# Kernel optimization log

Measured on AMD Instinct MI355X. Metric: run time of the kernel, lower is better.

Reference implementation:

```python
import jax, jax.numpy as jnp
import numpy as np

N = 100_000
E = 1_600_000
H = 128
F_NODE = 8
F_EDGE = 4
STEPS = 6
LN_EPS = 1e-6


def _ln(x, scale, bias):
    m = x.mean(-1, keepdims=True)
    v = ((x - m) ** 2).mean(-1, keepdims=True)
    return (x - m) * jax.lax.rsqrt(v + LN_EPS) * scale + bias


def setup_inputs() -> dict:
    key = jax.random.key(0)
    ks = iter(jax.random.split(key, 40))

    def rn(shape, scale=0.05):
        return jax.random.normal(next(ks), shape, jnp.float32) * scale

    inp = dict(
        node_feats=jax.random.normal(next(ks), (N, F_NODE), jnp.float32),
        edge_index=jax.random.randint(next(ks), (2, E), 0, N, jnp.int32),
        edge_feats=jax.random.normal(next(ks), (E, F_EDGE), jnp.float32),
        # input projection
        W_in=rn((F_NODE, H)), b_in=jnp.zeros((H,), jnp.float32),
        # per-step message MLP (distinct params each mp step -> leading axis STEPS)
        W_m1=rn((STEPS, 2 * H + F_EDGE, H)), b_m1=jnp.zeros((STEPS, H), jnp.float32),
        W_m2=rn((STEPS, H, H)), b_m2=jnp.zeros((STEPS, H), jnp.float32),
        # per-step GRU-style gates
        W_z=rn((STEPS, 2 * H, H)), b_z=jnp.zeros((STEPS, H), jnp.float32),
        W_r=rn((STEPS, 2 * H, H)), b_r=jnp.zeros((STEPS, H), jnp.float32),
        W_h=rn((STEPS, 2 * H, H)), b_h=jnp.zeros((STEPS, H), jnp.float32),
        # per-step LayerNorm
        ln_scale=jnp.ones((STEPS, H), jnp.float32), ln_bias=jnp.zeros((STEPS, H), jnp.float32),
        # classification head
        W_c1=rn((H, 64)), b_c1=jnp.zeros((64,), jnp.float32),
        W_c2=rn((64, 5)), b_c2=jnp.zeros((5,), jnp.float32),
        # collapse probability head
        W_p1=rn((H, 64)), b_p1=jnp.zeros((64,), jnp.float32),
        W_p2=rn((64, 1)), b_p2=jnp.zeros((1,), jnp.float32),
    )
    return inp


def reference(node_feats, edge_index, edge_feats, W_in, b_in,
              W_m1, b_m1, W_m2, b_m2, W_z, b_z, W_r, b_r, W_h, b_h,
              ln_scale, ln_bias, W_c1, b_c1, W_c2, b_c2, W_p1, b_p1, W_p2, b_p2):
    src, dst = edge_index[0], edge_index[1]
    h = node_feats @ W_in + b_in  # [N, H]
    n = h.shape[0]
    for s in range(STEPS):
        msg_in = jnp.concatenate([h[src], h[dst], edge_feats], axis=-1)  # [E, 2H+4]
        msg = jax.nn.relu(msg_in @ W_m1[s] + b_m1[s]) @ W_m2[s] + b_m2[s]  # [E, H]
        agg = jnp.zeros((n, H), h.dtype).at[dst].add(msg)  # [N, H]
        gate_in = jnp.concatenate([h, agg], axis=-1)  # [N, 2H]
        z = jax.nn.sigmoid(gate_in @ W_z[s] + b_z[s])
        r = jax.nn.sigmoid(gate_in @ W_r[s] + b_r[s])
        h_new = jnp.tanh(jnp.concatenate([r * h, agg], axis=-1) @ W_h[s] + b_h[s])
        h = _ln((1 - z) * h + z * h_new, ln_scale[s], ln_bias[s])
    cls = jax.nn.relu(h @ W_c1 + b_c1) @ W_c2 + b_c2  # [N, 5]
    prob = jax.nn.sigmoid(jax.nn.relu(h @ W_p1 + b_p1) @ W_p2 + b_p2).squeeze(-1)  # [N]
    return cls, prob
```

## Files before the change

kernel.cpp:

```cpp
#include <hip/hip_runtime.h>

#define STEPS 6

typedef __attribute__((ext_vector_type(8))) short short8;
typedef __attribute__((ext_vector_type(4))) float f32x4;
typedef __attribute__((ext_vector_type(8))) float f32x8;

__device__ __forceinline__ float bf2f(unsigned int u16) {
    union { unsigned int u; float f; } v; v.u = u16 << 16; return v.f;
}
__device__ __forceinline__ unsigned int f2bf(float x) {
    union { float f; unsigned int u; } v; v.f = x;
    unsigned int r = v.u + 0x7fffu + ((v.u >> 16) & 1u);
    return r >> 16;
}
__device__ __forceinline__ void decompv(const f32x8& v, short8& hi, short8& lo) {
#pragma unroll
    for (int j = 0; j < 8; ++j) {
        float x = v[j];
        unsigned int h = f2bf(x);
        hi[j] = (short)h;
        lo[j] = (short)f2bf(x - bf2f(h));
    }
}
__device__ __forceinline__ void gl_lds16(const void* g, void* s) {
    __builtin_amdgcn_global_load_lds(
        (const __attribute__((address_space(1))) unsigned int*)g,
        (__attribute__((address_space(3))) unsigned int*)s, 16, 0, 0);
}

__global__ __launch_bounds__(256) void hist_k(const int* __restrict__ dst, int* __restrict__ deg, int E) {
    int e = blockIdx.x * 256 + threadIdx.x;
    if (e < E) atomicAdd(&deg[dst[e]], 1);
}

__global__ __launch_bounds__(256) void scan1_k(const int* __restrict__ in, int* __restrict__ ex,
                                               int* __restrict__ bs, int N) {
    __shared__ int sd[256];
    int t = threadIdx.x;
    int base = blockIdx.x * 1024 + t * 4;
    int v[4]; int s = 0;
#pragma unroll
    for (int i = 0; i < 4; ++i) { int idx = base + i; v[i] = idx < N ? in[idx] : 0; s += v[i]; }
    sd[t] = s; __syncthreads();
    for (int o = 1; o < 256; o <<= 1) {
        int x = (t >= o) ? sd[t - o] : 0;
        __syncthreads();
        sd[t] += x;
        __syncthreads();
    }
    int run = sd[t] - s;
#pragma unroll
    for (int i = 0; i < 4; ++i) { int idx = base + i; if (idx < N) ex[idx] = run; run += v[i]; }
    if (t == 255) bs[blockIdx.x] = sd[255];
}

__global__ __launch_bounds__(1024) void scan2_k(const int* __restrict__ bs, int* __restrict__ be, int nb) {
    __shared__ int sd[1024];
    int t = threadIdx.x;
    int v = (t < nb) ? bs[t] : 0;
    sd[t] = v; __syncthreads();
    for (int o = 1; o < 1024; o <<= 1) {
        int x = (t >= o) ? sd[t - o] : 0;
        __syncthreads();
        sd[t] += x;
        __syncthreads();
    }
    if (t < nb) be[t] = sd[t] - v;
}

__global__ __launch_bounds__(256) void scan3_k(const int* __restrict__ ex, const int* __restrict__ be,
                                               int* __restrict__ offs, int N, int E) {
    int i = blockIdx.x * 256 + threadIdx.x;
    if (i < N) offs[i] = ex[i] + be[i >> 10];
    if (i == N) offs[N] = E;
}

__global__ __launch_bounds__(256) void scatter_k(const int* __restrict__ src, const int* __restrict__ dst,
                                                 const float4* __restrict__ ef,
                                                 const int* __restrict__ offs,
                                                 int* __restrict__ cursor, int* __restrict__ src_sorted,
                                                 uint2* __restrict__ ef16_sorted, int E) {
    int e = blockIdx.x * 256 + threadIdx.x;
    if (e >= E) return;
    int d = dst[e];
    int pos = offs[d] + atomicAdd(&cursor[d], 1);
    src_sorted[pos] = src[e];
    float4 f = ef[e];
    uint2 p;
    p.x = f2bf(f.x) | (f2bf(f.y) << 16);
    p.y = f2bf(f.z) | (f2bf(f.w) << 16);
    ef16_sorted[pos] = p;
}

__global__ __launch_bounds__(256) void pack_k(const float* __restrict__ W_m1, const float* __restrict__ W_m2,
                                              const float* __restrict__ W_z, const float* __restrict__ W_r,
                                              const float* __restrict__ W_h, unsigned short* __restrict__ packed) {
    const int s = blockIdx.y, mat = blockIdx.z;
    const int t = blockIdx.x * 256 + threadIdx.x;
    const int lane = t & 63;
    int KS, width; size_t moff;
    if (mat == 0)      { KS = 4; width = 256; moff = 0; }
    else if (mat == 1) { KS = 4; width = 128; moff = 32768; }
    else if (mat == 2) { KS = 8; width = 128; moff = 49152; }
    else if (mat == 3) { KS = 8; width = 128; moff = 81920; }
    else               { KS = 8; width = 128; moff = 114688; }
    const int total = (width >> 4) * KS * 64;
    if (t >= total) return;
    const int ks = (t >> 6) % KS;
    const int ct = (t >> 6) / KS;
    const int col = ct * 16 + (lane & 15);
    const int kb = ks * 32 + (lane >> 4) * 8;
    unsigned short* dh = packed + (size_t)s * 294912 + moff;
    unsigned short* dl = dh + 147456;
#pragma unroll
    for (int j = 0; j < 8; ++j) {
        const int k = kb + j;
        float v;
        if (mat == 0) {
            const float* W = W_m1 + (size_t)s * 260 * 128;
            v = (col < 128) ? W[k * 128 + col] : W[(128 + k) * 128 + (col - 128)];
        } else if (mat == 1) {
            v = W_m2[(size_t)s * 16384 + k * 128 + col];
        } else if (mat == 2) {
            v = W_z[(size_t)s * 32768 + k * 128 + col];
        } else if (mat == 3) {
            v = W_r[(size_t)s * 32768 + k * 128 + col];
        } else {
            v = W_h[(size_t)s * 32768 + k * 128 + col];
        }
        unsigned int hb = f2bf(v);
        dh[(size_t)t * 8 + j] = (unsigned short)hb;
        dl[(size_t)t * 8 + j] = (unsigned short)f2bf(v - bf2f(hb));
    }
}

__global__ __launch_bounds__(256) void pack_head_k(const float* __restrict__ Wc1,
                                                   const float* __restrict__ Wp1,
                                                   unsigned short* __restrict__ dst) {
    const int t = blockIdx.x * 256 + threadIdx.x;
    if (t >= 2048) return;
    const int lane = t & 63;
    const int ks = (t >> 6) & 3;
    const int ct = (t >> 6) >> 2;
    const int col = ct * 16 + (lane & 15);
    const int kb = ks * 32 + (lane >> 4) * 8;
    unsigned short* dh = dst;
    unsigned short* dl = dst + 16384;
#pragma unroll
    for (int j = 0; j < 8; ++j) {
        const int k = kb + j;
        float v = (col < 64) ? Wc1[k * 64 + col] : Wp1[k * 64 + (col - 64)];
        unsigned int hb = f2bf(v);
        dh[(size_t)t * 8 + j] = (unsigned short)hb;
        dl[(size_t)t * 8 + j] = (unsigned short)f2bf(v - bf2f(hb));
    }
}

__global__ __launch_bounds__(256) void proj_k(const float* __restrict__ nf, const float* __restrict__ Win,
                                              const float* __restrict__ bin,
                                              float* __restrict__ hf, int N) {
    const int lane = threadIdx.x & 63, wave = threadIdx.x >> 6;
    const int i = blockIdx.x * 4 + wave;
    if (i >= N) return;
    const int c0 = lane * 2;
    float a0 = bin[c0], a1 = bin[c0 + 1];
#pragma unroll
    for (int q = 0; q < 8; ++q) {
        float x = nf[(size_t)i * 8 + q];
        a0 += x * Win[q * 128 + c0];
        a1 += x * Win[q * 128 + c0 + 1];
    }
    hf[(size_t)i * 128 + c0] = a0;
    hf[(size_t)i * 128 + c0 + 1] = a1;
}

template <int MODE>
__global__ __launch_bounds__(256, 4) void gemm_k(const float* __restrict__ A, int lda,
                                                 const unsigned short* __restrict__ pkh,
                                                 const unsigned short* __restrict__ pkl,
                                                 const float* __restrict__ bias,
                                                 const int* __restrict__ deg,
                                                 float* __restrict__ out, int ldo,
                                                 unsigned short* __restrict__ out_b,
                                                 int Nrows) {
    const int lane = threadIdx.x & 63;
    const int wave = threadIdx.x >> 6;
    const int l15 = lane & 15, l16 = lane >> 4;
    const int mrow = blockIdx.x * 64 + wave * 16;
    const int cgrp = blockIdx.y;

    int r0 = mrow + l15; if (r0 >= Nrows) r0 = 0;
    const float* ap = A + (size_t)r0 * lda;

    f32x4 acc[8];
#pragma unroll
    for (int ct = 0; ct < 8; ++ct) acc[ct] = (f32x4){0.f, 0.f, 0.f, 0.f};

    for (int ks = 0; ks < 4; ++ks) {
        const f32x8 av = *(const f32x8*)(ap + ks * 32 + l16 * 8);
        short8 ahi, alo;
        decompv(av, ahi, alo);
#pragma unroll
        for (int ct = 0; ct < 8; ++ct) {
            const size_t fb = (((size_t)(cgrp * 8 + ct) * 4 + ks) << 10) + lane * 16;
            const short8 wh = *(const short8*)((const char*)pkh + fb);
            const short8 wl = *(const short8*)((const char*)pkl + fb);
            acc[ct] = __builtin_amdgcn_mfma_f32_16x16x32_bf16(ahi, wh, acc[ct], 0, 0, 0);
            acc[ct] = __builtin_amdgcn_mfma_f32_16x16x32_bf16(alo, wh, acc[ct], 0, 0, 0);
            acc[ct] = __builtin_amdgcn_mfma_f32_16x16x32_bf16(ahi, wl, acc[ct], 0, 0, 0);
        }
    }
#pragma unroll
    for (int ct = 0; ct < 8; ++ct) {
        const int col = cgrp * 128 + ct * 16 + l15;
#pragma unroll
        for (int r = 0; r < 4; ++r) {
            const int row = mrow + l16 * 4 + r;
            if (row >= Nrows) continue;
            float v = acc[ct][r];
            if (MODE == 0) {
                if (cgrp == 0) out_b[(size_t)row * 128 + col] = (unsigned short)f2bf(v);
                else           out[(size_t)row * ldo + col] = v;
            } else {
                v += bias[col] * (float)deg[row];
                out[(size_t)row * ldo + col] = v;
            }
        }
    }
}

__global__ __launch_bounds__(512, 4) void zrh_k(float* __restrict__ hf,
                                                const float* __restrict__ X,
                                                const unsigned short* __restrict__ pzh, const unsigned short* __restrict__ pzl,
                                                const unsigned short* __restrict__ prh, const unsigned short* __restrict__ prl,
                                                const unsigned short* __restrict__ phh, const unsigned short* __restrict__ phl,
                                                const float* __restrict__ bz, const float* __restrict__ br,
                                                const float* __restrict__ bh,
                                                const float* __restrict__ lns, const float* __restrict__ lnb,
                                                int N) {
    __shared__ char stg[49152];
    float* rhs = reinterpret_cast<float*>(stg);
    float* lnp = reinterpret_cast<float*>(stg + 33792);
    const int lane = threadIdx.x & 63;
    const int wave = threadIdx.x >> 6;
    const int rowgrp = wave >> 1, colgrp = wave & 1;
    const int l15 = lane & 15, l16 = lane >> 4;
    const int mrow = blockIdx.x * 64 + rowgrp * 16;

    int r0 = mrow + l15; if (r0 >= N) r0 = 0;

    f32x4 zac[4], rac[4], hac[4];
#pragma unroll
    for (int c = 0; c < 4; ++c) {
        zac[c] = (f32x4){0.f, 0.f, 0.f, 0.f};
        rac[c] = (f32x4){0.f, 0.f, 0.f, 0.f};
        hac[c] = (f32x4){0.f, 0.f, 0.f, 0.f};
    }

    const unsigned short* wsrc[6] = {pzh, pzl, prh, prl, phh, phl};

    f32x8 acur = *(const f32x8*)(hf + (size_t)r0 * 128 + l16 * 8);
    for (int ks = 0; ks < 8; ++ks) {
        const int nplanes = (ks >= 4) ? 6 : 4;
        for (int i = 0; i < nplanes; ++i)
            gl_lds16((const char*)wsrc[i] + (((size_t)(wave * 8 + ks)) << 10) + lane * 16,
                     &stg[(i * 8 + wave) << 10]);
        f32x8 anext;
        if (ks < 7) {
            const int kn = (ks + 1) * 32 + l16 * 8;
            const float* ap = (kn < 128) ? (hf + (size_t)r0 * 128 + kn)
                                         : (X + (size_t)r0 * 256 + (kn - 128));
            f32x4 pa = *(const f32x4*)ap;
            f32x4 pb = *(const f32x4*)(ap + 4);
            anext[0] = pa[0]; anext[1] = pa[1]; anext[2] = pa[2]; anext[3] = pa[3];
            anext[4] = pb[0]; anext[5] = pb[1]; anext[6] = pb[2]; anext[7] = pb[3];
        }
        short8 ahi, alo;
        decompv(acur, ahi, alo);
        if (ks < 7) asm volatile("s_waitcnt vmcnt(2)" ::: "memory");
        else        asm volatile("s_waitcnt vmcnt(0)" ::: "memory");
        __builtin_amdgcn_sched_barrier(0);
        __builtin_amdgcn_s_barrier();
        __builtin_amdgcn_sched_barrier(0);
#pragma unroll
        for (int c = 0; c < 4; ++c) {
            const int ct = colgrp * 4 + c;
            const short8 wzh = *(const short8*)(stg + ((0 * 8 + ct) << 10) + lane * 16);
            const short8 wzl = *(const short8*)(stg + ((1 * 8 + ct) << 10) + lane * 16);
            const short8 wrh = *(const short8*)(stg + ((2 * 8 + ct) << 10) + lane * 16);
            const short8 wrl = *(const short8*)(stg + ((3 * 8 + ct) << 10) + lane * 16);
            zac[c] = __builtin_amdgcn_mfma_f32_16x16x32_bf16(ahi, wzh, zac[c], 0, 0, 0);
            zac[c] = __builtin_amdgcn_mfma_f32_16x16x32_bf16(alo, wzh, zac[c], 0, 0, 0);
            zac[c] = __builtin_amdgcn_mfma_f32_16x16x32_bf16(ahi, wzl, zac[c], 0, 0, 0);
            rac[c] = __builtin_amdgcn_mfma_f32_16x16x32_bf16(ahi, wrh, rac[c], 0, 0, 0);
            rac[c] = __builtin_amdgcn_mfma_f32_16x16x32_bf16(alo, wrh, rac[c], 0, 0, 0);
            rac[c] = __builtin_amdgcn_mfma_f32_16x16x32_bf16(ahi, wrl, rac[c], 0, 0, 0);
            if (ks >= 4) {
                const short8 wbh = *(const short8*)(stg + ((4 * 8 + ct) << 10) + lane * 16);
                const short8 wbl = *(const short8*)(stg + ((5 * 8 + ct) << 10) + lane * 16);
                hac[c] = __builtin_amdgcn_mfma_f32_16x16x32_bf16(ahi, wbh, hac[c], 0, 0, 0);
                hac[c] = __builtin_amdgcn_mfma_f32_16x16x32_bf16(alo, wbh, hac[c], 0, 0, 0);
                hac[c] = __builtin_amdgcn_mfma_f32_16x16x32_bf16(ahi, wbl, hac[c], 0, 0, 0);
            }
        }
        __builtin_amdgcn_sched_barrier(0);
        __builtin_amdgcn_s_barrier();
        acur = anext;
    }

#pragma unroll
    for (int c = 0; c < 4; ++c) {
        const int col = (colgrp * 4 + c) * 16 + l15;
#pragma unroll
        for (int r = 0; r < 4; ++r) {
            const int rowl = l16 * 4 + r;
            const int row = mrow + rowl;
            const size_t idx = (size_t)(row < N ? row : 0) * 128 + col;
            float zp = zac[c][r] + bz[col];
            zac[c][r] = 1.f / (1.f + expf(-zp));
            float rp = rac[c][r] + br[col];
            float rr = 1.f / (1.f + expf(-rp));
            rhs[rowgrp * 2112 + rowl * 132 + col] = rr * hf[idx];
        }
    }
    __syncthreads();

    for (int ks = 0; ks < 4; ++ks) {
        const f32x8 v = *(const f32x8*)(rhs + rowgrp * 2112 + l15 * 132 + (ks * 4 + l16) * 8);
        short8 ahi, alo;
        decompv(v, ahi, alo);
#pragma unroll
        for (int c = 0; c < 4; ++c) {
            const int ct = colgrp * 4 + c;
            const size_t fb = (((size_t)(ct * 8 + ks)) << 10) + lane * 16;
            const short8 wh = *(const short8*)((const char*)phh + fb);
            const short8 wl = *(const short8*)((const char*)phl + fb);
            hac[c] = __builtin_amdgcn_mfma_f32_16x16x32_bf16(ahi, wh, hac[c], 0, 0, 0);
            hac[c] = __builtin_amdgcn_mfma_f32_16x16x32_bf16(alo, wh, hac[c], 0, 0, 0);
            hac[c] = __builtin_amdgcn_mfma_f32_16x16x32_bf16(ahi, wl, hac[c], 0, 0, 0);
        }
    }

#pragma unroll
    for (int c = 0; c < 4; ++c) {
        const int col = (colgrp * 4 + c) * 16 + l15;
#pragma unroll
        for (int r = 0; r < 4; ++r) {
            const int row = mrow + l16 * 4 + r;
            const size_t idx = (size_t)(row < N ? row : 0) * 128 + col;
            float hn = tanhf(hac[c][r] + bh[col]);
            float zz = zac[c][r];
            hac[c][r] = (1.f - zz) * hf[idx] + zz * hn;
        }
    }
    float sr[4], ssr[4];
#pragma unroll
    for (int r = 0; r < 4; ++r) {
        float s = 0.f, ss = 0.f;
#pragma unroll
        for (int c = 0; c < 4; ++c) {
            float y = hac[c][r];
            s += y; ss += y * y;
        }
#pragma unroll
        for (int m = 1; m < 16; m <<= 1) {
            s += __shfl_xor(s, m, 64);
            ss += __shfl_xor(ss, m, 64);
        }
        sr[r] = s; ssr[r] = ss;
        if (l15 == 0) {
            float* p = lnp + (((rowgrp * 2 + colgrp) * 16) + (l16 * 4 + r)) * 2;
            p[0] = s; p[1] = ss;
        }
    }
    __syncthreads();
#pragma unroll
    for (int r = 0; r < 4; ++r) {
        const int rowl = l16 * 4 + r;
        const int row = mrow + rowl;
        const float* po = lnp + (((rowgrp * 2 + (colgrp ^ 1)) * 16) + rowl) * 2;
        float s = sr[r] + po[0];
        float ss = ssr[r] + po[1];
        float mean = s * (1.f / 128.f);
        float var = ss * (1.f / 128.f) - mean * mean;
        float inv = rsqrtf(var + 1e-6f);
        if (row < N) {
#pragma unroll
            for (int c = 0; c < 4; ++c) {
                const int col = (colgrp * 4 + c) * 16 + l15;
                hf[(size_t)row * 128 + col] = (hac[c][r] - mean) * inv * lns[col] + lnb[col];
            }
        }
    }
}

__global__ __launch_bounds__(256) void edge_k(float* __restrict__ X,
                                              const unsigned short* __restrict__ Xs16,
                                              const int* __restrict__ offs,
                                              const int* __restrict__ src_sorted,
                                              const uint2* __restrict__ ef16_sorted,
                                              const float* __restrict__ Wm1_s,
                                              const float* __restrict__ bm1_s,
                                              int N) {
    const int lane = threadIdx.x & 63, wave = threadIdx.x >> 6;
    const int v = blockIdx.x * 4 + wave;
    if (v >= N) return;
    const int c0 = lane * 2;
    const float base0 = X[(size_t)v * 256 + 128 + c0] + bm1_s[c0];
    const float base1 = X[(size_t)v * 256 + 129 + c0] + bm1_s[c0 + 1];
    const float w0x = Wm1_s[256 * 128 + c0], w0y = Wm1_s[256 * 128 + c0 + 1];
    const float w1x = Wm1_s[257 * 128 + c0], w1y = Wm1_s[257 * 128 + c0 + 1];
    const float w2x = Wm1_s[258 * 128 + c0], w2y = Wm1_s[258 * 128 + c0 + 1];
    const float w3x = Wm1_s[259 * 128 + c0], w3y = Wm1_s[259 * 128 + c0 + 1];
    float acc0 = 0.f, acc1 = 0.f;
    const int beg = offs[v], end = offs[v + 1];
    int i = beg;
    for (; i + 3 < end; i += 4) {
        int sn0 = src_sorted[i], sn1 = src_sorted[i + 1];
        int sn2 = src_sorted[i + 2], sn3 = src_sorted[i + 3];
        uint2 ep0 = ef16_sorted[i], ep1 = ef16_sorted[i + 1];
        uint2 ep2 = ef16_sorted[i + 2], ep3 = ef16_sorted[i + 3];
        unsigned int xs0 = *reinterpret_cast<const unsigned int*>(Xs16 + (size_t)sn0 * 128 + c0);
        unsigned int xs1 = *reinterpret_cast<const unsigned int*>(Xs16 + (size_t)sn1 * 128 + c0);
        unsigned int xs2 = *reinterpret_cast<const unsigned int*>(Xs16 + (size_t)sn2 * 128 + c0);
        unsigned int xs3 = *reinterpret_cast<const unsigned int*>(Xs16 + (size_t)sn3 * 128 + c0);
        {
            float efa = bf2f(ep0.x & 0xffffu), efb = bf2f(ep0.x >> 16);
            float efc = bf2f(ep0.y & 0xffffu), efd = bf2f(ep0.y >> 16);
            float e0 = efa * w0x + efb * w1x + efc * w2x + efd * w3x;
            float e1 = efa * w0y + efb * w1y + efc * w2y + efd * w3y;
            acc0 += fmaxf(bf2f(xs0 & 0xffffu) + base0 + e0, 0.f);
            acc1 += fmaxf(bf2f(xs0 >> 16) + base1 + e1, 0.f);
        }
        {
            float efa = bf2f(ep1.x & 0xffffu), efb = bf2f(ep1.x >> 16);
            float efc = bf2f(ep1.y & 0xffffu), efd = bf2f(ep1.y >> 16);
            float e0 = efa * w0x + efb * w1x + efc * w2x + efd * w3x;
            float e1 = efa * w0y + efb * w1y + efc * w2y + efd * w3y;
            acc0 += fmaxf(bf2f(xs1 & 0xffffu) + base0 + e0, 0.f);
            acc1 += fmaxf(bf2f(xs1 >> 16) + base1 + e1, 0.f);
        }
        {
            float efa = bf2f(ep2.x & 0xffffu), efb = bf2f(ep2.x >> 16);
            float efc = bf2f(ep2.y & 0xffffu), efd = bf2f(ep2.y >> 16);
            float e0 = efa * w0x + efb * w1x + efc * w2x + efd * w3x;
            float e1 = efa * w0y + efb * w1y + efc * w2y + efd * w3y;
            acc0 += fmaxf(bf2f(xs2 & 0xffffu) + base0 + e0, 0.f);
            acc1 += fmaxf(bf2f(xs2 >> 16) + base1 + e1, 0.f);
        }
        {
            float efa = bf2f(ep3.x & 0xffffu), efb = bf2f(ep3.x >> 16);
            float efc = bf2f(ep3.y & 0xffffu), efd = bf2f(ep3.y >> 16);
            float e0 = efa * w0x + efb * w1x + efc * w2x + efd * w3x;
            float e1 = efa * w0y + efb * w1y + efc * w2y + efd * w3y;
            acc0 += fmaxf(bf2f(xs3 & 0xffffu) + base0 + e0, 0.f);
            acc1 += fmaxf(bf2f(xs3 >> 16) + base1 + e1, 0.f);
        }
    }
    for (; i < end; ++i) {
        int sn = src_sorted[i];
        uint2 efp = ef16_sorted[i];
        float efa = bf2f(efp.x & 0xffffu), efb = bf2f(efp.x >> 16);
        float efc = bf2f(efp.y & 0xffffu), efd = bf2f(efp.y >> 16);
        unsigned int xs = *reinterpret_cast<const unsigned int*>(Xs16 + (size_t)sn * 128 + c0);
        float e0 = efa * w0x + efb * w1x + efc * w2x + efd * w3x;
        float e1 = efa * w0y + efb * w1y + efc * w2y + efd * w3y;
        acc0 += fmaxf(bf2f(xs & 0xffffu) + base0 + e0, 0.f);
        acc1 += fmaxf(bf2f(xs >> 16) + base1 + e1, 0.f);
    }
    X[(size_t)v * 256 + 128 + c0] = acc0;
    X[(size_t)v * 256 + 129 + c0] = acc1;
}

__global__ __launch_bounds__(256, 4) void head_k(const float* __restrict__ hf,
                                                 const unsigned short* __restrict__ pH,
                                                 const float* __restrict__ bc1, const float* __restrict__ bp1,
                                                 const float* __restrict__ Wc2, const float* __restrict__ bc2,
                                                 const float* __restrict__ Wp2, const float* __restrict__ bp2,
                                                 float* __restrict__ out, int N) {
    __shared__ float tls[4][16][132];
    const int lane = threadIdx.x & 63, wave = threadIdx.x >> 6;
    const int l15 = lane & 15, l16 = lane >> 4;
    const int mrow = blockIdx.x * 64 + wave * 16;
    const unsigned short* pHl = pH + 16384;

    int r0 = mrow + l15; if (r0 >= N) r0 = 0;
    const float* ap = hf + (size_t)r0 * 128;

    f32x4 acc[8];
#pragma unroll
    for (int ct = 0; ct < 8; ++ct) acc[ct] = (f32x4){0.f, 0.f, 0.f, 0.f};

    for (int ks = 0; ks < 4; ++ks) {
        const f32x8 av = *(const f32x8*)(ap + ks * 32 + l16 * 8);
        short8 ahi, alo;
        decompv(av, ahi, alo);
#pragma unroll
        for (int ct = 0; ct < 8; ++ct) {
            const size_t fb = (((size_t)(ct * 4 + ks)) << 10) + lane * 16;
            const short8 wh = *(const short8*)((const char*)pH + fb);
            const short8 wl = *(const short8*)((const char*)pHl + fb);
            acc[ct] = __builtin_amdgcn_mfma_f32_16x16x32_bf16(ahi, wh, acc[ct], 0, 0, 0);
            acc[ct] = __builtin_amdgcn_mfma_f32_16x16x32_bf16(alo, wh, acc[ct], 0, 0, 0);
            acc[ct] = __builtin_amdgcn_mfma_f32_16x16x32_bf16(ahi, wl, acc[ct], 0, 0, 0);
        }
    }
#pragma unroll
    for (int ct = 0; ct < 8; ++ct) {
        const int col = ct * 16 + l15;
        const float b = (col < 64) ? bc1[col] : bp1[col - 64];
#pragma unroll
        for (int r = 0; r < 4; ++r) {
            const int rowl = l16 * 4 + r;
            tls[wave][rowl][col] = fmaxf(acc[ct][r] + b, 0.f);
        }
    }
    const int rowl = lane & 15;
    const int g = lane >> 4;
    const int row = mrow + rowl;
    const float* tr = &tls[wave][rowl][0];
    float o0 = 0.f, o1 = 0.f;
    if (g == 0) {
        for (int k = 0; k < 64; ++k) { float tv = tr[k]; o0 += tv * Wc2[k * 5 + 0]; o1 += tv * Wc2[k * 5 + 4]; }
    } else if (g == 1) {
        for (int k = 0; k < 64; ++k) { o0 += tr[k] * Wc2[k * 5 + 1]; o1 += tr[64 + k] * Wp2[k]; }
    } else if (g == 2) {
        for (int k = 0; k < 64; ++k) o0 += tr[k] * Wc2[k * 5 + 2];
    } else {
        for (int k = 0; k < 64; ++k) o0 += tr[k] * Wc2[k * 5 + 3];
    }
    if (row < N) {
        if (g == 0) {
            out[(size_t)row * 5 + 0] = o0 + bc2[0];
            out[(size_t)row * 5 + 4] = o1 + bc2[4];
        } else if (g == 1) {
            out[(size_t)row * 5 + 1] = o0 + bc2[1];
            out[(size_t)N * 5 + row] = 1.f / (1.f + expf(-(o1 + bp2[0])));
        } else if (g == 2) {
            out[(size_t)row * 5 + 2] = o0 + bc2[2];
        } else {
            out[(size_t)row * 5 + 3] = o0 + bc2[3];
        }
    }
}

extern "C" void kernel_launch(void* const* d_in, const int* in_sizes, int n_in,
                              void* d_out, int out_size, void* d_ws, size_t ws_size,
                              hipStream_t stream) {
    const float* node_feats = (const float*)d_in[0];
    const int*   edge_index = (const int*)d_in[1];
    const float* edge_feats = (const float*)d_in[2];
    const float* W_in = (const float*)d_in[3];
    const float* b_in = (const float*)d_in[4];
    const float* W_m1 = (const float*)d_in[5];
    const float* b_m1 = (const float*)d_in[6];
    const float* W_m2 = (const float*)d_in[7];
    const float* b_m2 = (const float*)d_in[8];
    const float* W_z  = (const float*)d_in[9];
    const float* b_z  = (const float*)d_in[10];
    const float* W_r  = (const float*)d_in[11];
    const float* b_r  = (const float*)d_in[12];
    const float* W_h  = (const float*)d_in[13];
    const float* b_h  = (const float*)d_in[14];
    const float* ln_s = (const float*)d_in[15];
    const float* ln_b = (const float*)d_in[16];
    const float* W_c1 = (const float*)d_in[17];
    const float* b_c1 = (const float*)d_in[18];
    const float* W_c2 = (const float*)d_in[19];
    const float* b_c2 = (const float*)d_in[20];
    const float* W_p1 = (const float*)d_in[21];
    const float* b_p1 = (const float*)d_in[22];
    const float* W_p2 = (const float*)d_in[23];
    const float* b_p2 = (const float*)d_in[24];

    const int N = in_sizes[0] / 8;
    const int E = in_sizes[2] / 4;

    char* ws = (char*)d_ws;
    size_t off = 0;
    auto alloc = [&](size_t bytes) { size_t p = off; off = (off + bytes + 255) & ~(size_t)255; return p; };
    const size_t o_hf = alloc((size_t)N * 128 * 4);
    const size_t o_X  = alloc((size_t)N * 256 * 4);
    const size_t o_xs = alloc((size_t)N * 128 * 2);
    const size_t o_pk = alloc(((size_t)STEPS * 294912 + 32768) * 2);
    const size_t o_deg = alloc((size_t)N * 4);
    const size_t o_off = alloc((size_t)(N + 1) * 4);
    const size_t o_cur = alloc((size_t)N * 4);
    const size_t o_ex  = alloc((size_t)N * 4);
    const size_t o_bs  = alloc(1024 * 4);
    const size_t o_be  = alloc(1024 * 4);
    const size_t o_ss  = alloc((size_t)E * 4);
    const size_t o_ef  = alloc((size_t)E * 8);

    if (off > ws_size) {
        hipMemsetAsync(d_out, 0, (size_t)out_size * 4, stream);
        return;
    }

    float* hf = (float*)(ws + o_hf);
    float* X  = (float*)(ws + o_X);
    unsigned short* Xs16 = (unsigned short*)(ws + o_xs);
    unsigned short* pH = (unsigned short*)(ws + o_pk) + (size_t)STEPS * 294912;

    hipMemsetAsync(ws + o_deg, 0, (size_t)N * 4, stream);
    hipMemsetAsync(ws + o_cur, 0, (size_t)N * 4, stream);
    hist_k<<<(E + 255) / 256, 256, 0, stream>>>(edge_index + E, (int*)(ws + o_deg), E);
    const int nb1 = (N + 1023) / 1024;
    scan1_k<<<nb1, 256, 0, stream>>>((int*)(ws + o_deg), (int*)(ws + o_ex), (int*)(ws + o_bs), N);
    scan2_k<<<1, 1024, 0, stream>>>((int*)(ws + o_bs), (int*)(ws + o_be), nb1);
    scan3_k<<<(N + 1 + 255) / 256, 256, 0, stream>>>((int*)(ws + o_ex), (int*)(ws + o_be),
                                                     (int*)(ws + o_off), N, E);
    scatter_k<<<(E + 255) / 256, 256, 0, stream>>>(edge_index, edge_index + E,
                                                   (const float4*)edge_feats, (int*)(ws + o_off),
                                                   (int*)(ws + o_cur), (int*)(ws + o_ss),
                                                   (uint2*)(ws + o_ef), E);
    pack_k<<<dim3(16, STEPS, 5), 256, 0, stream>>>(W_m1, W_m2, W_z, W_r, W_h,
                                                   (unsigned short*)(ws + o_pk));
    pack_head_k<<<8, 256, 0, stream>>>(W_c1, W_p1, pH);
    proj_k<<<(N + 3) / 4, 256, 0, stream>>>(node_feats, W_in, b_in, hf, N);

    const int MB2 = (N + 63) / 64;

    for (int s = 0; s < STEPS; ++s) {
        const unsigned short* pk = (const unsigned short*)(ws + o_pk) + (size_t)s * 294912;
        const unsigned short* pkL = pk + 147456;
        gemm_k<0><<<dim3(MB2, 2), 256, 0, stream>>>(hf, 128, pk, pkL, nullptr, nullptr,
                                                    X, 256, Xs16, N);
        edge_k<<<(N + 3) / 4, 256, 0, stream>>>(X, Xs16, (int*)(ws + o_off), (int*)(ws + o_ss),
                                                (const uint2*)(ws + o_ef),
                                                W_m1 + (size_t)s * 33280, b_m1 + (size_t)s * 128, N);
        gemm_k<1><<<dim3(MB2, 1), 256, 0, stream>>>(X + 128, 256, pk + 32768, pkL + 32768,
                                                    b_m2 + (size_t)s * 128, (int*)(ws + o_deg),
                                                    X, 256, nullptr, N);
        zrh_k<<<MB2, 512, 0, stream>>>(hf, X,
                                       pk + 49152, pkL + 49152,
                                       pk + 81920, pkL + 81920,
                                       pk + 114688, pkL + 114688,
                                       b_z + (size_t)s * 128, b_r + (size_t)s * 128,
                                       b_h + (size_t)s * 128,
                                       ln_s + (size_t)s * 128, ln_b + (size_t)s * 128, N);
    }

    head_k<<<MB2, 256, 0, stream>>>(hf, pH, b_c1, b_p1, W_c2, b_c2, W_p2, b_p2,
                                    (float*)d_out, N);
}
```

Measured before the change: 2.039 ms.

## Store activations as packed bf16 hi/lo pairs to skip per-load decomposition

```diff
diff --git a/kernel.cpp b/kernel.cpp
--- a/kernel.cpp
+++ b/kernel.cpp
@@ -5,6 +5,7 @@
 typedef __attribute__((ext_vector_type(8))) short short8;
 typedef __attribute__((ext_vector_type(4))) float f32x4;
 typedef __attribute__((ext_vector_type(8))) float f32x8;
+typedef __attribute__((ext_vector_type(8))) unsigned int u32x8;
 
 __device__ __forceinline__ float bf2f(unsigned int u16) {
     union { unsigned int u; float f; } v; v.u = u16 << 16; return v.f;
@@ -14,13 +15,19 @@
     unsigned int r = v.u + 0x7fffu + ((v.u >> 16) & 1u);
     return r >> 16;
 }
-__device__ __forceinline__ void decompv(const f32x8& v, short8& hi, short8& lo) {
+__device__ __forceinline__ unsigned int packhl(float x) {
+    unsigned int h = f2bf(x);
+    unsigned int l = f2bf(x - bf2f(h));
+    return (h & 0xffffu) | (l << 16);
+}
+__device__ __forceinline__ float unpackf(unsigned int u) {
+    return bf2f(u & 0xffffu) + bf2f(u >> 16);
+}
+__device__ __forceinline__ void unpackv(const u32x8& a, short8& hi, short8& lo) {
 #pragma unroll
     for (int j = 0; j < 8; ++j) {
-        float x = v[j];
-        unsigned int h = f2bf(x);
-        hi[j] = (short)h;
-        lo[j] = (short)f2bf(x - bf2f(h));
+        hi[j] = (short)(a[j] & 0xffffu);
+        lo[j] = (short)(a[j] >> 16);
     }
 }
 __device__ __forceinline__ void gl_lds16(const void* g, void* s) {
@@ -159,7 +166,7 @@
 
 __global__ __launch_bounds__(256) void proj_k(const float* __restrict__ nf, const float* __restrict__ Win,
                                               const float* __restrict__ bin,
-                                              float* __restrict__ hf, int N) {
+                                              unsigned int* __restrict__ h2, int N) {
     const int lane = threadIdx.x & 63, wave = threadIdx.x >> 6;
     const int i = blockIdx.x * 4 + wave;
     if (i >= N) return;
@@ -171,17 +178,18 @@
         a0 += x * Win[q * 128 + c0];
         a1 += x * Win[q * 128 + c0 + 1];
     }
-    hf[(size_t)i * 128 + c0] = a0;
-    hf[(size_t)i * 128 + c0 + 1] = a1;
+    h2[(size_t)i * 128 + c0] = packhl(a0);
+    h2[(size_t)i * 128 + c0 + 1] = packhl(a1);
 }
 
 template <int MODE>
-__global__ __launch_bounds__(256, 4) void gemm_k(const float* __restrict__ A, int lda,
+__global__ __launch_bounds__(256, 4) void gemm_k(const unsigned int* __restrict__ A, int lda,
                                                  const unsigned short* __restrict__ pkh,
                                                  const unsigned short* __restrict__ pkl,
                                                  const float* __restrict__ bias,
                                                  const int* __restrict__ deg,
-                                                 float* __restrict__ out, int ldo,
+                                                 float* __restrict__ outf,
+                                                 unsigned int* __restrict__ outu,
                                                  unsigned short* __restrict__ out_b,
                                                  int Nrows) {
     const int lane = threadIdx.x & 63;
@@ -191,16 +199,16 @@
     const int cgrp = blockIdx.y;
 
     int r0 = mrow + l15; if (r0 >= Nrows) r0 = 0;
-    const float* ap = A + (size_t)r0 * lda;
+    const unsigned int* ap = A + (size_t)r0 * lda;
 
     f32x4 acc[8];
 #pragma unroll
     for (int ct = 0; ct < 8; ++ct) acc[ct] = (f32x4){0.f, 0.f, 0.f, 0.f};
 
     for (int ks = 0; ks < 4; ++ks) {
-        const f32x8 av = *(const f32x8*)(ap + ks * 32 + l16 * 8);
+        const u32x8 av = *(const u32x8*)(ap + ks * 32 + l16 * 8);
         short8 ahi, alo;
-        decompv(av, ahi, alo);
+        unpackv(av, ahi, alo);
 #pragma unroll
         for (int ct = 0; ct < 8; ++ct) {
             const size_t fb = (((size_t)(cgrp * 8 + ct) * 4 + ks) << 10) + lane * 16;
@@ -221,17 +229,17 @@
             float v = acc[ct][r];
             if (MODE == 0) {
                 if (cgrp == 0) out_b[(size_t)row * 128 + col] = (unsigned short)f2bf(v);
-                else           out[(size_t)row * ldo + col] = v;
+                else           outf[(size_t)row * 256 + col] = v;
             } else {
                 v += bias[col] * (float)deg[row];
-                out[(size_t)row * ldo + col] = v;
+                outu[(size_t)row * 256 + col] = packhl(v);
             }
         }
     }
 }
 
-__global__ __launch_bounds__(512, 4) void zrh_k(float* __restrict__ hf,
-                                                const float* __restrict__ X,
+__global__ __launch_bounds__(512, 4) void zrh_k(unsigned int* __restrict__ h2,
+                                                const unsigned int* __restrict__ Xu,
                                                 const unsigned short* __restrict__ pzh, const unsigned short* __restrict__ pzl,
                                                 const unsigned short* __restrict__ prh, const unsigned short* __restrict__ prl,
                                                 const unsigned short* __restrict__ phh, const unsigned short* __restrict__ phl,
@@ -240,7 +248,7 @@
                                                 const float* __restrict__ lns, const float* __restrict__ lnb,
                                                 int N) {
     __shared__ char stg[49152];
-    float* rhs = reinterpret_cast<float*>(stg);
+    unsigned int* rhs = reinterpret_cast<unsigned int*>(stg);
     float* lnp = reinterpret_cast<float*>(stg + 33792);
     const int lane = threadIdx.x & 63;
     const int wave = threadIdx.x >> 6;
@@ -260,25 +268,22 @@
 
     const unsigned short* wsrc[6] = {pzh, pzl, prh, prl, phh, phl};
 
-    f32x8 acur = *(const f32x8*)(hf + (size_t)r0 * 128 + l16 * 8);
+    u32x8 acur = *(const u32x8*)(h2 + (size_t)r0 * 128 + l16 * 8);
     for (int ks = 0; ks < 8; ++ks) {
         const int nplanes = (ks >= 4) ? 6 : 4;
         for (int i = 0; i < nplanes; ++i)
             gl_lds16((const char*)wsrc[i] + (((size_t)(wave * 8 + ks)) << 10) + lane * 16,
                      &stg[(i * 8 + wave) << 10]);
-        f32x8 anext;
+        u32x8 anext;
         if (ks < 7) {
             const int kn = (ks + 1) * 32 + l16 * 8;
-            const float* ap = (kn < 128) ? (hf + (size_t)r0 * 128 + kn)
-                                         : (X + (size_t)r0 * 256 + (kn - 128));
-            f32x4 pa = *(const f32x4*)ap;
-            f32x4 pb = *(const f32x4*)(ap + 4);
-            anext[0] = pa[0]; anext[1] = pa[1]; anext[2] = pa[2]; anext[3] = pa[3];
-            anext[4] = pb[0]; anext[5] = pb[1]; anext[6] = pb[2]; anext[7] = pb[3];
+            const unsigned int* ap = (kn < 128) ? (h2 + (size_t)r0 * 128 + kn)
+                                                : (Xu + (size_t)r0 * 256 + (kn - 128));
+            anext = *(const u32x8*)ap;
         }
         short8 ahi, alo;
-        decompv(acur, ahi, alo);
-        if (ks < 7) asm volatile("s_waitcnt vmcnt(2)" ::: "memory");
+        unpackv(acur, ahi, alo);
+        if (ks < 7) asm volatile("s_waitcnt vmcnt(1)" ::: "memory");
         else        asm volatile("s_waitcnt vmcnt(0)" ::: "memory");
         __builtin_amdgcn_sched_barrier(0);
         __builtin_amdgcn_s_barrier();
@@ -321,15 +326,15 @@
             zac[c][r] = 1.f / (1.f + expf(-zp));
             float rp = rac[c][r] + br[col];
             float rr = 1.f / (1.f + expf(-rp));
-            rhs[rowgrp * 2112 + rowl * 132 + col] = rr * hf[idx];
+            rhs[rowgrp * 2112 + rowl * 132 + col] = packhl(rr * unpackf(h2[idx]));
         }
     }
     __syncthreads();
 
     for (int ks = 0; ks < 4; ++ks) {
-        const f32x8 v = *(const f32x8*)(rhs + rowgrp * 2112 + l15 * 132 + (ks * 4 + l16) * 8);
+        const u32x8 v = *(const u32x8*)(rhs + rowgrp * 2112 + l15 * 132 + (ks * 4 + l16) * 8);
         short8 ahi, alo;
-        decompv(v, ahi, alo);
+        unpackv(v, ahi, alo);
 #pragma unroll
         for (int c = 0; c < 4; ++c) {
             const int ct = colgrp * 4 + c;
@@ -351,7 +356,7 @@
             const size_t idx = (size_t)(row < N ? row : 0) * 128 + col;
             float hn = tanhf(hac[c][r] + bh[col]);
             float zz = zac[c][r];
-            hac[c][r] = (1.f - zz) * hf[idx] + zz * hn;
+            hac[c][r] = (1.f - zz) * unpackf(h2[idx]) + zz * hn;
         }
     }
     float sr[4], ssr[4];
@@ -389,13 +394,14 @@
 #pragma unroll
             for (int c = 0; c < 4; ++c) {
                 const int col = (colgrp * 4 + c) * 16 + l15;
-                hf[(size_t)row * 128 + col] = (hac[c][r] - mean) * inv * lns[col] + lnb[col];
+                h2[(size_t)row * 128 + col] = packhl((hac[c][r] - mean) * inv * lns[col] + lnb[col]);
             }
         }
     }
 }
 
 __global__ __launch_bounds__(256) void edge_k(float* __restrict__ X,
+                                              unsigned int* __restrict__ Xu,
                                               const unsigned short* __restrict__ Xs16,
                                               const int* __restrict__ offs,
                                               const int* __restrict__ src_sorted,
@@ -469,11 +475,11 @@
         acc0 += fmaxf(bf2f(xs & 0xffffu) + base0 + e0, 0.f);
         acc1 += fmaxf(bf2f(xs >> 16) + base1 + e1, 0.f);
     }
-    X[(size_t)v * 256 + 128 + c0] = acc0;
-    X[(size_t)v * 256 + 129 + c0] = acc1;
-}
-
-__global__ __launch_bounds__(256, 4) void head_k(const float* __restrict__ hf,
+    Xu[(size_t)v * 256 + 128 + c0] = packhl(acc0);
+    Xu[(size_t)v * 256 + 129 + c0] = packhl(acc1);
+}
+
+__global__ __launch_bounds__(256, 4) void head_k(const unsigned int* __restrict__ h2,
                                                  const unsigned short* __restrict__ pH,
                                                  const float* __restrict__ bc1, const float* __restrict__ bp1,
                                                  const float* __restrict__ Wc2, const float* __restrict__ bc2,
@@ -486,16 +492,16 @@
     const unsigned short* pHl = pH + 16384;
 
     int r0 = mrow + l15; if (r0 >= N) r0 = 0;
-    const float* ap = hf + (size_t)r0 * 128;
+    const unsigned int* ap = h2 + (size_t)r0 * 128;
 
     f32x4 acc[8];
 #pragma unroll
     for (int ct = 0; ct < 8; ++ct) acc[ct] = (f32x4){0.f, 0.f, 0.f, 0.f};
 
     for (int ks = 0; ks < 4; ++ks) {
-        const f32x8 av = *(const f32x8*)(ap + ks * 32 + l16 * 8);
+        const u32x8 av = *(const u32x8*)(ap + ks * 32 + l16 * 8);
         short8 ahi, alo;
-        decompv(av, ahi, alo);
+        unpackv(av, ahi, alo);
 #pragma unroll
         for (int ct = 0; ct < 8; ++ct) {
             const size_t fb = (((size_t)(ct * 4 + ks)) << 10) + lane * 16;
@@ -580,7 +586,7 @@
     char* ws = (char*)d_ws;
     size_t off = 0;
     auto alloc = [&](size_t bytes) { size_t p = off; off = (off + bytes + 255) & ~(size_t)255; return p; };
-    const size_t o_hf = alloc((size_t)N * 128 * 4);
+    const size_t o_h2 = alloc((size_t)N * 128 * 4);
     const size_t o_X  = alloc((size_t)N * 256 * 4);
     const size_t o_xs = alloc((size_t)N * 128 * 2);
     const size_t o_pk = alloc(((size_t)STEPS * 294912 + 32768) * 2);
@@ -598,8 +604,9 @@
         return;
     }
 
-    float* hf = (float*)(ws + o_hf);
+    unsigned int* h2 = (unsigned int*)(ws + o_h2);
     float* X  = (float*)(ws + o_X);
+    unsigned int* Xu = (unsigned int*)(ws + o_X);
     unsigned short* Xs16 = (unsigned short*)(ws + o_xs);
     unsigned short* pH = (unsigned short*)(ws + o_pk) + (size_t)STEPS * 294912;
 
@@ -618,22 +625,22 @@
     pack_k<<<dim3(16, STEPS, 5), 256, 0, stream>>>(W_m1, W_m2, W_z, W_r, W_h,
                                                    (unsigned short*)(ws + o_pk));
     pack_head_k<<<8, 256, 0, stream>>>(W_c1, W_p1, pH);
-    proj_k<<<(N + 3) / 4, 256, 0, stream>>>(node_feats, W_in, b_in, hf, N);
+    proj_k<<<(N + 3) / 4, 256, 0, stream>>>(node_feats, W_in, b_in, h2, N);
 
     const int MB2 = (N + 63) / 64;
 
     for (int s = 0; s < STEPS; ++s) {
         const unsigned short* pk = (const unsigned short*)(ws + o_pk) + (size_t)s * 294912;
         const unsigned short* pkL = pk + 147456;
-        gemm_k<0><<<dim3(MB2, 2), 256, 0, stream>>>(hf, 128, pk, pkL, nullptr, nullptr,
-                                                    X, 256, Xs16, N);
-        edge_k<<<(N + 3) / 4, 256, 0, stream>>>(X, Xs16, (int*)(ws + o_off), (int*)(ws + o_ss),
+        gemm_k<0><<<dim3(MB2, 2), 256, 0, stream>>>(h2, 128, pk, pkL, nullptr, nullptr,
+                                                    X, nullptr, Xs16, N);
+        edge_k<<<(N + 3) / 4, 256, 0, stream>>>(X, Xu, Xs16, (int*)(ws + o_off), (int*)(ws + o_ss),
                                                 (const uint2*)(ws + o_ef),
                                                 W_m1 + (size_t)s * 33280, b_m1 + (size_t)s * 128, N);
-        gemm_k<1><<<dim3(MB2, 1), 256, 0, stream>>>(X + 128, 256, pk + 32768, pkL + 32768,
+        gemm_k<1><<<dim3(MB2, 1), 256, 0, stream>>>(Xu + 128, 256, pk + 32768, pkL + 32768,
                                                     b_m2 + (size_t)s * 128, (int*)(ws + o_deg),
-                                                    X, 256, nullptr, N);
-        zrh_k<<<MB2, 512, 0, stream>>>(hf, X,
+                                                    nullptr, Xu, nullptr, N);
+        zrh_k<<<MB2, 512, 0, stream>>>(h2, Xu,
                                        pk + 49152, pkL + 49152,
                                        pk + 81920, pkL + 81920,
                                        pk + 114688, pkL + 114688,
@@ -642,6 +649,6 @@
                                        ln_s + (size_t)s * 128, ln_b + (size_t)s * 128, N);
     }
 
-    head_k<<<MB2, 256, 0, stream>>>(hf, pH, b_c1, b_p1, W_c2, b_c2, W_p2, b_p2,
+    head_k<<<MB2, 256, 0, stream>>>(h2, pH, b_c1, b_p1, W_c2, b_c2, W_p2, b_p2,
                                     (float*)d_out, N);
 }
```

Result: slower. 2.162 ms (+6.0%).
